# Kernel optimization log

Measured on AMD Instinct MI355X. Metric: run time of the kernel, lower is better.

Reference implementation:

```python
import jax, jax.numpy as jnp
import numpy as np

B, L, H, O, C = 64, 32, 128, 16384, 32


def setup_inputs() -> dict:
    key = jax.random.key(0)
    ks = jax.random.split(key, 8)
    s = lambda k, shp, fan: jax.random.normal(k, shp, jnp.float32) / np.sqrt(fan)
    return {
        "z": jax.random.normal(ks[0], (B, L), jnp.float32),
        "feature_embedding": jax.random.normal(ks[1], (O, C), jnp.float32),
        "feature_bias": jax.random.normal(ks[2], (O, 1), jnp.float32),
        "Wz": s(ks[3], (L, H), L),
        "bz": jnp.zeros((H,), jnp.float32),
        "W1": s(ks[4], (H + C + 1, H), H + C + 1),
        "b1": jnp.zeros((H,), jnp.float32),
        "W2": s(ks[5], (H, 1), H),
        "b2": jnp.zeros((1,), jnp.float32),
    }


def reference(z, feature_embedding, feature_bias, Wz, bz, W1, b1, W2, b2):
    # z_processor: Linear + ReLU (dropout_rate=0)
    pz = jax.nn.relu(z @ Wz + bz)  # [B, H]
    # concat([pz, F, b], -1) @ W1  ==  pz@W1_h + F@W1_f + b*W1_b  (no [B,O,H+C+1] materialization)
    W1_h, W1_f, W1_b = W1[:H], W1[H:H + C], W1[H + C:]  # [H,H],[C,H],[1,H]
    h = jax.nn.relu(
        (pz @ W1_h)[:, None, :]                    # [B,1,H]
        + (feature_embedding @ W1_f)[None, :, :]   # [1,O,H]
        + feature_bias * W1_b                      # [O,H] broadcast
        + b1
    )  # [B, O, H]
    out = jnp.einsum("boh,ho->bo", h, W2) + b2  # [B, O]
    return out
```

## Files before the change

kernel.cpp:

```cpp
#include <hip/hip_runtime.h>

#define Bb 64
#define Ll 32
#define Hh 128
#define Oo 16384
#define Cc 32
#define TOo 64
#define NT 1024

__device__ __forceinline__ float rdlane(float v, int l) {
    return __int_as_float(__builtin_amdgcn_readlane(__float_as_int(v), l));
}

__global__ __launch_bounds__(256) void prep_kernel(
    const float* __restrict__ z, const float* __restrict__ Wz,
    const float* __restrict__ bz, const float* __restrict__ W1,
    const float* __restrict__ W2,
    float* __restrict__ A, float* __restrict__ SA2w)
{
    __shared__ float pz[2][Hh];
    __shared__ float ps[2][Hh];
    const int t  = threadIdx.x;
    const int h  = t & (Hh - 1);
    const int bb = t >> 7;
    const int b  = blockIdx.x * 2 + bb;

    float v = bz[h];
#pragma unroll
    for (int c = 0; c < Ll; ++c)
        v = fmaf(z[b * Ll + c], Wz[c * Hh + h], v);
    pz[bb][h] = fmaxf(v, 0.f);
    __syncthreads();

    float a = 0.f;
#pragma unroll
    for (int k = 0; k < Hh; ++k)
        a = fmaf(pz[bb][k], W1[k * Hh + h], a);
    A[b * Hh + h] = a;
    ps[bb][h] = 0.5f * W2[h] * a;
    __syncthreads();

    if (h == 0) {
        float s = 0.f;
        for (int k = 0; k < Hh; ++k) s += ps[bb][k];
        SA2w[b] = s;
    }
}

__global__ __launch_bounds__(NT) void main_kernel(
    const float* __restrict__ A,  const float* __restrict__ SA2w,
    const float* __restrict__ fe, const float* __restrict__ fb,
    const float* __restrict__ W1, const float* __restrict__ b1,
    const float* __restrict__ W2, const float* __restrict__ b2,
    float* __restrict__ out)
{
    __shared__ float gT[Hh][TOo + 1];
    __shared__ float part[4][Bb][TOo];

    const int t    = threadIdx.x;
    const int o0   = blockIdx.x * TOo;
    const int lane = t & 63;
    const int wave = __builtin_amdgcn_readfirstlane(t >> 6);

    const int hh = wave & 3, bg = wave >> 2;
    const int h0 = hh * 32,  b0 = bg * 16;

    const int bi_l = lane >> 2, hc_l = lane & 3;
    const float* Ap = A + (b0 + bi_l) * Hh + h0 + hc_l * 8;
    const float4 av_lo = *(const float4*)(Ap);
    const float4 av_hi = *(const float4*)(Ap + 4);

    {
        const int hG = ((wave & 1) << 6) + lane;
        const int og = wave >> 1;
        const int ol = lane >> 3, ccl = lane & 7;
        const float4 fe4 = *(const float4*)(fe + (o0 + og * 8 + ol) * Cc + ccl * 4);

        float w1f[Cc];
#pragma unroll
        for (int c = 0; c < Cc; ++c)
            w1f[c] = W1[(Hh + c) * Hh + hG];
        const float w1b = W1[(Hh + Cc) * Hh + hG];
        const float b1h = b1[hG];

#pragma unroll
        for (int j = 0; j < 8; ++j) {
            float g = fmaf(fb[o0 + og * 8 + j], w1b, b1h);
#pragma unroll
            for (int c2 = 0; c2 < 8; ++c2) {
                const int L = j * 8 + c2;
                g = fmaf(rdlane(fe4.x, L), w1f[c2 * 4 + 0], g);
                g = fmaf(rdlane(fe4.y, L), w1f[c2 * 4 + 1], g);
                g = fmaf(rdlane(fe4.z, L), w1f[c2 * 4 + 2], g);
                g = fmaf(rdlane(fe4.w, L), w1f[c2 * 4 + 3], g);
            }
            gT[hG][og * 8 + j] = g;
        }
    }
    __syncthreads();

    float gv[32];
#pragma unroll
    for (int k = 0; k < 32; ++k)
        gv[k] = gT[h0 + k][lane];

    const float w2l = 0.5f * W2[h0 + (lane & 31)];
    float w2v[32];
#pragma unroll
    for (int k = 0; k < 32; ++k)
        w2v[k] = rdlane(w2l, k);

    float sg = 0.f;
#pragma unroll
    for (int k = 0; k < 32; ++k)
        sg = fmaf(w2v[k], gv[k], sg);

    float acc[16];
#pragma unroll
    for (int bi = 0; bi < 16; ++bi) acc[bi] = sg;

#pragma unroll
    for (int jc = 0; jc < 8; ++jc) {
        const float4 a4s = (jc & 1) ? av_hi : av_lo;
        const float g0 = gv[4 * jc + 0], g1 = gv[4 * jc + 1];
        const float g2 = gv[4 * jc + 2], g3 = gv[4 * jc + 3];
        const float u0 = w2v[4 * jc + 0], u1 = w2v[4 * jc + 1];
        const float u2 = w2v[4 * jc + 2], u3 = w2v[4 * jc + 3];
#pragma unroll
        for (int bi = 0; bi < 16; ++bi) {
            const int L = bi * 4 + (jc >> 1);
            acc[bi] = fmaf(__builtin_fabsf(rdlane(a4s.x, L) + g0), u0, acc[bi]);
            acc[bi] = fmaf(__builtin_fabsf(rdlane(a4s.y, L) + g1), u1, acc[bi]);
            acc[bi] = fmaf(__builtin_fabsf(rdlane(a4s.z, L) + g2), u2, acc[bi]);
            acc[bi] = fmaf(__builtin_fabsf(rdlane(a4s.w, L) + g3), u3, acc[bi]);
        }
    }

#pragma unroll
    for (int bi = 0; bi < 16; ++bi)
        part[hh][b0 + bi][lane] = acc[bi];
    __syncthreads();

    const float b2v = b2[0];
#pragma unroll
    for (int q = 0; q < 4; ++q) {
        const int b = wave * 4 + q;
        const float r = part[0][b][lane] + part[1][b][lane]
                      + part[2][b][lane] + part[3][b][lane];
        out[b * Oo + o0 + lane] = r + SA2w[b] + b2v;
    }
}

extern "C" void kernel_launch(void* const* d_in, const int* in_sizes, int n_in,
                              void* d_out, int out_size, void* d_ws, size_t ws_size,
                              hipStream_t stream) {
    (void)in_sizes; (void)n_in; (void)out_size; (void)ws_size;
    const float* z   = (const float*)d_in[0];
    const float* fe  = (const float*)d_in[1];
    const float* fb  = (const float*)d_in[2];
    const float* Wz  = (const float*)d_in[3];
    const float* bz  = (const float*)d_in[4];
    const float* W1  = (const float*)d_in[5];
    const float* b1  = (const float*)d_in[6];
    const float* W2  = (const float*)d_in[7];
    const float* b2  = (const float*)d_in[8];
    float* out  = (float*)d_out;
    float* A    = (float*)d_ws;
    float* SA2w = A + Bb * Hh;

    prep_kernel<<<Bb / 2, 256, 0, stream>>>(z, Wz, bz, W1, W2, A, SA2w);
    main_kernel<<<Oo / TOo, NT, 0, stream>>>(A, SA2w, fe, fb, W1, b1, W2, b2, out);
}
```

Baseline: 92.21 us.

## Restructure main kernel to use uniform scalar weight loads instead of readlane broadcasts

New measurement: 96.66 us. 4.8% more time.

```diff
diff --git a/kernel.cpp b/kernel.cpp
--- a/kernel.cpp
+++ b/kernel.cpp
@@ -6,17 +6,17 @@
 #define Oo 16384
 #define Cc 32
 #define TOo 64
-#define NT 1024
+#define NT 512
 
-__device__ __forceinline__ float rdlane(float v, int l) {
-    return __int_as_float(__builtin_amdgcn_readlane(__float_as_int(v), l));
-}
 
 __global__ __launch_bounds__(256) void prep_kernel(
     const float* __restrict__ z, const float* __restrict__ Wz,
     const float* __restrict__ bz, const float* __restrict__ W1,
-    const float* __restrict__ W2,
-    float* __restrict__ A, float* __restrict__ SA2w)
+    const float* __restrict__ b1, const float* __restrict__ W2,
+    const float* __restrict__ b2,
+    float* __restrict__ A, float* __restrict__ SA2w,
+    float* __restrict__ w2h, float* __restrict__ w1t,
+    float* __restrict__ gcoef)
 {
     __shared__ float pz[2][Hh];
     __shared__ float ps[2][Hh];
@@ -41,113 +41,101 @@
     __syncthreads();
 
     if (h == 0) {
-        float s = 0.f;
+        float s = b2[0];
         for (int k = 0; k < Hh; ++k) s += ps[bb][k];
         SA2w[b] = s;
+    }
+
+    if (t < 128) {
+        const int h2 = blockIdx.x * 4 + (t >> 5);
+        const int c  = t & 31;
+        w1t[h2 * Cc + c] = W1[(Hh + c) * Hh + h2];
+    }
+    if (t < 4) {
+        const int h2 = blockIdx.x * 4 + t;
+        w2h[h2] = 0.5f * W2[h2];
+        gcoef[2 * h2 + 0] = W1[(Hh + Cc) * Hh + h2];
+        gcoef[2 * h2 + 1] = b1[h2];
     }
 }
 
 __global__ __launch_bounds__(NT) void main_kernel(
-    const float* __restrict__ A,  const float* __restrict__ SA2w,
-    const float* __restrict__ fe, const float* __restrict__ fb,
-    const float* __restrict__ W1, const float* __restrict__ b1,
-    const float* __restrict__ W2, const float* __restrict__ b2,
-    float* __restrict__ out)
+    const float* __restrict__ A,   const float* __restrict__ SA2w,
+    const float* __restrict__ fe,  const float* __restrict__ fb,
+    const float* __restrict__ w2h, const float* __restrict__ w1t,
+    const float* __restrict__ gcoef, float* __restrict__ out)
 {
-    __shared__ float gT[Hh][TOo + 1];
-    __shared__ float part[4][Bb][TOo];
+    __shared__ __align__(16) float fe_s[TOo][36];
+    __shared__ float g_s[Hh][TOo + 1];
 
     const int t    = threadIdx.x;
     const int o0   = blockIdx.x * TOo;
     const int lane = t & 63;
     const int wave = __builtin_amdgcn_readfirstlane(t >> 6);
 
-    const int hh = wave & 3, bg = wave >> 2;
-    const int h0 = hh * 32,  b0 = bg * 16;
-
-    const int bi_l = lane >> 2, hc_l = lane & 3;
-    const float* Ap = A + (b0 + bi_l) * Hh + h0 + hc_l * 8;
-    const float4 av_lo = *(const float4*)(Ap);
-    const float4 av_hi = *(const float4*)(Ap + 4);
-
     {
-        const int hG = ((wave & 1) << 6) + lane;
-        const int og = wave >> 1;
-        const int ol = lane >> 3, ccl = lane & 7;
-        const float4 fe4 = *(const float4*)(fe + (o0 + og * 8 + ol) * Cc + ccl * 4);
-
-        float w1f[Cc];
-#pragma unroll
-        for (int c = 0; c < Cc; ++c)
-            w1f[c] = W1[(Hh + c) * Hh + hG];
-        const float w1b = W1[(Hh + Cc) * Hh + hG];
-        const float b1h = b1[hG];
-
-#pragma unroll
-        for (int j = 0; j < 8; ++j) {
-            float g = fmaf(fb[o0 + og * 8 + j], w1b, b1h);
-#pragma unroll
-            for (int c2 = 0; c2 < 8; ++c2) {
-                const int L = j * 8 + c2;
-                g = fmaf(rdlane(fe4.x, L), w1f[c2 * 4 + 0], g);
-                g = fmaf(rdlane(fe4.y, L), w1f[c2 * 4 + 1], g);
-                g = fmaf(rdlane(fe4.z, L), w1f[c2 * 4 + 2], g);
-                g = fmaf(rdlane(fe4.w, L), w1f[c2 * 4 + 3], g);
-            }
-            gT[hG][og * 8 + j] = g;
-        }
+        const float4 f4 = ((const float4*)(fe + o0 * Cc))[t];
+        *(float4*)&fe_s[t >> 3][(t & 7) << 2] = f4;
     }
     __syncthreads();
 
-    float gv[32];
+    float4 fer[8];
 #pragma unroll
-    for (int k = 0; k < 32; ++k)
-        gv[k] = gT[h0 + k][lane];
+    for (int k = 0; k < 8; ++k)
+        fer[k] = *(const float4*)&fe_s[lane][4 * k];
+    const float fbv = fb[o0 + lane];
 
-    const float w2l = 0.5f * W2[h0 + (lane & 31)];
-    float w2v[32];
+    const int h0 = wave * 16;
+#pragma unroll 1
+    for (int j = 0; j < 16; ++j) {
+        const int h = h0 + j;
+        const float w1b = gcoef[2 * h + 0];
+        const float b1h = gcoef[2 * h + 1];
+        const float* __restrict__ wt = w1t + h * Cc;
+        float g = fmaf(fbv, w1b, b1h);
 #pragma unroll
-    for (int k = 0; k < 32; ++k)
-        w2v[k] = rdlane(w2l, k);
+        for (int k = 0; k < 8; ++k) {
+            g = fmaf(fer[k].x, wt[4 * k + 0], g);
+            g = fmaf(fer[k].y, wt[4 * k + 1], g);
+            g = fmaf(fer[k].z, wt[4 * k + 2], g);
+            g = fmaf(fer[k].w, wt[4 * k + 3], g);
+        }
+        g_s[h][lane] = g;
+    }
+    __syncthreads();
 
+    const int b0 = wave * 8;
+    float acc[8];
+#pragma unroll
+    for (int bi = 0; bi < 8; ++bi) acc[bi] = 0.f;
     float sg = 0.f;
+
+#pragma unroll 1
+    for (int tt = 0; tt < 8; ++tt) {
+        float gj[16];
 #pragma unroll
-    for (int k = 0; k < 32; ++k)
-        sg = fmaf(w2v[k], gv[k], sg);
-
-    float acc[16];
+        for (int jr = 0; jr < 16; ++jr)
+            gj[jr] = g_s[16 * tt + jr][lane];
+        const float* __restrict__ wp = w2h + 16 * tt;
+        float w[16];
 #pragma unroll
-    for (int bi = 0; bi < 16; ++bi) acc[bi] = sg;
-
+        for (int jr = 0; jr < 16; ++jr) w[jr] = wp[jr];
 #pragma unroll
-    for (int jc = 0; jc < 8; ++jc) {
-        const float4 a4s = (jc & 1) ? av_hi : av_lo;
-        const float g0 = gv[4 * jc + 0], g1 = gv[4 * jc + 1];
-        const float g2 = gv[4 * jc + 2], g3 = gv[4 * jc + 3];
-        const float u0 = w2v[4 * jc + 0], u1 = w2v[4 * jc + 1];
-        const float u2 = w2v[4 * jc + 2], u3 = w2v[4 * jc + 3];
+        for (int jr = 0; jr < 16; ++jr)
+            sg = fmaf(w[jr], gj[jr], sg);
 #pragma unroll
-        for (int bi = 0; bi < 16; ++bi) {
-            const int L = bi * 4 + (jc >> 1);
-            acc[bi] = fmaf(__builtin_fabsf(rdlane(a4s.x, L) + g0), u0, acc[bi]);
-            acc[bi] = fmaf(__builtin_fabsf(rdlane(a4s.y, L) + g1), u1, acc[bi]);
-            acc[bi] = fmaf(__builtin_fabsf(rdlane(a4s.z, L) + g2), u2, acc[bi]);
-            acc[bi] = fmaf(__builtin_fabsf(rdlane(a4s.w, L) + g3), u3, acc[bi]);
+        for (int bi = 0; bi < 8; ++bi) {
+            const float* __restrict__ Ap = A + (b0 + bi) * Hh + 16 * tt;
+#pragma unroll
+            for (int jr = 0; jr < 16; ++jr)
+                acc[bi] = fmaf(__builtin_fabsf(gj[jr] + Ap[jr]), w[jr], acc[bi]);
         }
     }
 
 #pragma unroll
-    for (int bi = 0; bi < 16; ++bi)
-        part[hh][b0 + bi][lane] = acc[bi];
-    __syncthreads();
-
-    const float b2v = b2[0];
-#pragma unroll
-    for (int q = 0; q < 4; ++q) {
-        const int b = wave * 4 + q;
-        const float r = part[0][b][lane] + part[1][b][lane]
-                      + part[2][b][lane] + part[3][b][lane];
-        out[b * Oo + o0 + lane] = r + SA2w[b] + b2v;
+    for (int bi = 0; bi < 8; ++bi) {
+        const int b = b0 + bi;
+        out[b * Oo + o0 + lane] = acc[bi] + sg + SA2w[b];
     }
 }
 
@@ -164,10 +152,15 @@
     const float* b1  = (const float*)d_in[6];
     const float* W2  = (const float*)d_in[7];
     const float* b2  = (const float*)d_in[8];
-    float* out  = (float*)d_out;
-    float* A    = (float*)d_ws;
-    float* SA2w = A + Bb * Hh;
+    float* out   = (float*)d_out;
+    float* A     = (float*)d_ws;
+    float* SA2w  = A + Bb * Hh;
+    float* w2h   = SA2w + Bb;
+    float* w1t   = w2h + Hh;
+    float* gcoef = w1t + Hh * Cc;
 
-    prep_kernel<<<Bb / 2, 256, 0, stream>>>(z, Wz, bz, W1, W2, A, SA2w);
-    main_kernel<<<Oo / TOo, NT, 0, stream>>>(A, SA2w, fe, fb, W1, b1, W2, b2, out);
+    prep_kernel<<<Bb / 2, 256, 0, stream>>>(z, Wz, bz, W1, b1, W2, b2,
+                                            A, SA2w, w2h, w1t, gcoef);
+    main_kernel<<<Oo / TOo, NT, 0, stream>>>(A, SA2w, fe, fb, w2h, w1t,
+                                             gcoef, out);
 }
```
